# Kernel tuning notes

Measured on AMD Instinct MI355X. Metric: run time of the kernel, lower is better.

## Reference

```python
import jax, jax.numpy as jnp
import numpy as np

N_NODES = 100000
N_EDGES = 3200000
F_IN = 512
HIDDEN = 64
N_CLASSES = 64


def setup_inputs() -> dict:
    key = jax.random.key(0)
    ks = jax.random.split(key, 6)
    node_features = jax.random.normal(ks[0], (N_NODES, F_IN), dtype=jnp.float32)
    edge_rows = jax.random.randint(ks[1], (N_EDGES,), 0, N_NODES, dtype=jnp.int32)
    edge_cols = jax.random.randint(ks[2], (N_EDGES,), 0, N_NODES, dtype=jnp.int32)
    edge_vals = jax.random.uniform(ks[3], (N_EDGES,), dtype=jnp.float32)
    W1 = jax.random.normal(ks[4], (F_IN, HIDDEN), dtype=jnp.float32) / np.sqrt(F_IN)
    b1 = jnp.zeros((HIDDEN,), dtype=jnp.float32)
    W2 = jax.random.normal(ks[5], (HIDDEN, N_CLASSES), dtype=jnp.float32) / np.sqrt(HIDDEN)
    b2 = jnp.zeros((N_CLASSES,), dtype=jnp.float32)
    return {
        "node_features": node_features,
        "edge_rows": edge_rows,
        "edge_cols": edge_cols,
        "edge_vals": edge_vals,
        "W1": W1,
        "b1": b1,
        "W2": W2,
        "b2": b2,
    }


def reference(node_features, edge_rows, edge_cols, edge_vals, W1, b1, W2, b2):
    # MLP node transform (inference: dropout is identity, no norms)
    h = jax.nn.relu(node_features @ W1 + b1)          # [N, HIDDEN]
    logits = h @ W2 + b2                              # [N, C]
    # smoother @ logits : sparse [N,N] COO times dense [N,C]
    messages = edge_vals[:, None] * logits[edge_cols]  # [E, C]
    out = jax.ops.segment_sum(messages, edge_rows, num_segments=N_NODES)
    return out
```

## Files before the change

kernel.cpp:

```cpp
#include <hip/hip_runtime.h>
#include <hip/hip_bf16.h>
#include <stdint.h>

#define N_NODES 100000
#define N_EDGES 3200000
#define F_IN    512
#define HIDDEN  64
#define NCLS    64

#define BROWS   64
#define NBKT    1563
#define NBKT_PAD 1792
#define CHUNK   4096
#define CAP     2432
#define OVF_CAP 8192
#define SENTINEL ((int)0x80000000)

typedef float v4f __attribute__((ext_vector_type(4)));
typedef short v8s __attribute__((ext_vector_type(8)));

__device__ __forceinline__ unsigned short f2bf(float f){
  unsigned u = __float_as_uint(f);
  u += 0x7fffu + ((u >> 16) & 1u);
  return (unsigned short)(u >> 16);
}
__device__ __forceinline__ float bflo(unsigned u){ return __uint_as_float(u << 16); }
__device__ __forceinline__ float bfhi(unsigned u){ return __uint_as_float(u & 0xffff0000u); }

__global__ void prep_weights(const float* __restrict__ W1, const float* __restrict__ W2,
                             unsigned short* __restrict__ w1f, unsigned short* __restrict__ w2f,
                             int* __restrict__ zeroc){
  int t = blockIdx.x * 256 + threadIdx.x;
  if (t < NBKT*16 + 16) zeroc[t] = 0;
  if (t < 16*4*64*8){
    int j = t & 7, lane = (t >> 3) & 63, nt = (t >> 9) & 3, ks = t >> 11;
    int m = lane & 15, q = lane >> 4;
    int k = ks*32 + q*8 + j, n = nt*16 + m;
    w1f[t] = f2bf(W1[k*HIDDEN + n]);
  } else {
    int u = t - 16*4*64*8;
    if (u < 2*4*64*8){
      int j = u & 7, lane = (u >> 3) & 63, nt = (u >> 9) & 3, ks = u >> 11;
      int m = lane & 15, q = lane >> 4;
      int k = ks*32 + q*8 + j, n = nt*16 + m;
      w2f[u] = f2bf(W2[k*NCLS + n]);
    }
  }
}

__global__ __launch_bounds__(256) void mlp_kernel(
    const float* __restrict__ X, const float* __restrict__ b1,
    const float* __restrict__ b2,
    const unsigned short* __restrict__ w1f, const unsigned short* __restrict__ w2f,
    unsigned short* __restrict__ logits){
  __shared__ __align__(16) float lds[4][16][68];
  int tid  = threadIdx.x;
  int wid  = tid >> 6, lane = tid & 63;
  int m    = lane & 15, q = lane >> 4;
  int base = blockIdx.x * 64 + wid * 16;
  if (base > N_NODES - 16) base = N_NODES - 16;

  const float* rp = X + (size_t)(base + m) * F_IN + q * 8;
  const v8s* w1v = (const v8s*)w1f;
  const v8s* w2v = (const v8s*)w2f;

  v4f a0c = {0,0,0,0}, a1c = {0,0,0,0}, a2c = {0,0,0,0}, a3c = {0,0,0,0};
  #pragma unroll
  for (int ks = 0; ks < 16; ++ks){
    const float4* pa = (const float4*)(rp + ks * 32);
    float4 x0 = pa[0], x1 = pa[1];
    v8s af;
    af[0]=(short)f2bf(x0.x); af[1]=(short)f2bf(x0.y); af[2]=(short)f2bf(x0.z); af[3]=(short)f2bf(x0.w);
    af[4]=(short)f2bf(x1.x); af[5]=(short)f2bf(x1.y); af[6]=(short)f2bf(x1.z); af[7]=(short)f2bf(x1.w);
    a0c = __builtin_amdgcn_mfma_f32_16x16x32_bf16(af, w1v[(ks*4+0)*64 + lane], a0c, 0,0,0);
    a1c = __builtin_amdgcn_mfma_f32_16x16x32_bf16(af, w1v[(ks*4+1)*64 + lane], a1c, 0,0,0);
    a2c = __builtin_amdgcn_mfma_f32_16x16x32_bf16(af, w1v[(ks*4+2)*64 + lane], a2c, 0,0,0);
    a3c = __builtin_amdgcn_mfma_f32_16x16x32_bf16(af, w1v[(ks*4+3)*64 + lane], a3c, 0,0,0);
  }

  float b1v0 = b1[m], b1v1 = b1[16+m], b1v2 = b1[32+m], b1v3 = b1[48+m];
  #pragma unroll
  for (int r = 0; r < 4; ++r){
    int row = q*4 + r;
    lds[wid][row][     m] = fmaxf(a0c[r] + b1v0, 0.f);
    lds[wid][row][16 + m] = fmaxf(a1c[r] + b1v1, 0.f);
    lds[wid][row][32 + m] = fmaxf(a2c[r] + b1v2, 0.f);
    lds[wid][row][48 + m] = fmaxf(a3c[r] + b1v3, 0.f);
  }
  __syncthreads();

  v4f c0 = {0,0,0,0}, c1 = {0,0,0,0}, c2 = {0,0,0,0}, c3 = {0,0,0,0};
  #pragma unroll
  for (int k2 = 0; k2 < 2; ++k2){
    const float4* ph = (const float4*)&lds[wid][m][k2*32 + q*8];
    float4 h0 = ph[0], h1 = ph[1];
    v8s af;
    af[0]=(short)f2bf(h0.x); af[1]=(short)f2bf(h0.y); af[2]=(short)f2bf(h0.z); af[3]=(short)f2bf(h0.w);
    af[4]=(short)f2bf(h1.x); af[5]=(short)f2bf(h1.y); af[6]=(short)f2bf(h1.z); af[7]=(short)f2bf(h1.w);
    c0 = __builtin_amdgcn_mfma_f32_16x16x32_bf16(af, w2v[(k2*4+0)*64 + lane], c0, 0,0,0);
    c1 = __builtin_amdgcn_mfma_f32_16x16x32_bf16(af, w2v[(k2*4+1)*64 + lane], c1, 0,0,0);
    c2 = __builtin_amdgcn_mfma_f32_16x16x32_bf16(af, w2v[(k2*4+2)*64 + lane], c2, 0,0,0);
    c3 = __builtin_amdgcn_mfma_f32_16x16x32_bf16(af, w2v[(k2*4+3)*64 + lane], c3, 0,0,0);
  }

  float b2v0 = b2[m], b2v1 = b2[16+m], b2v2 = b2[32+m], b2v3 = b2[48+m];
  unsigned short* lp = logits + (size_t)base * NCLS;
  #pragma unroll
  for (int r = 0; r < 4; ++r){
    int row = q*4 + r;
    lp[row*NCLS +      m] = f2bf(c0[r] + b2v0);
    lp[row*NCLS + 16 + m] = f2bf(c1[r] + b2v1);
    lp[row*NCLS + 32 + m] = f2bf(c2[r] + b2v2);
    lp[row*NCLS + 48 + m] = f2bf(c3[r] + b2v3);
  }
}

__global__ __launch_bounds__(256) void bucket_scatter(
    const int* __restrict__ rows, const int* __restrict__ cols,
    const float* __restrict__ vals, int* __restrict__ bcur,
    int* __restrict__ ovf_cnt, int4* __restrict__ ovf,
    int2* __restrict__ ebkt){
  __shared__ int  lcnt[NBKT_PAD];
  __shared__ int  lbase[NBKT_PAD];
  __shared__ int  ssum[256];
  __shared__ int2 stage[CHUNK];
  __shared__ int  sdst[CHUNK];
  int t = threadIdx.x;
  int base = blockIdx.x * CHUNK;
  int cnt  = min(CHUNK, N_EDGES - base);

  #pragma unroll
  for (int i = 0; i < 7; ++i) lcnt[t*7 + i] = 0;
  __syncthreads();

  int r[16];
  #pragma unroll
  for (int k = 0; k < 16; ++k){
    int li = t + k*256;
    if (li < cnt){
      r[k] = rows[base + li];
      atomicAdd(&lcnt[r[k] >> 6], 1);
    } else r[k] = -1;
  }
  __syncthreads();

  int v[7]; int s = 0;
  #pragma unroll
  for (int k = 0; k < 7; ++k){ v[k] = lcnt[t*7 + k]; s += v[k]; }
  ssum[t] = s; __syncthreads();
  for (int o = 1; o < 256; o <<= 1){
    int add = (t >= o) ? ssum[t - o] : 0;
    __syncthreads();
    ssum[t] += add;
    __syncthreads();
  }
  int run = ssum[t] - s;
  #pragma unroll
  for (int k = 0; k < 7; ++k){
    int b = t*7 + k;
    if (b < NBKT){
      if (v[k]){
        int g = atomicAdd(&bcur[b*16], v[k]);
        lbase[b] = b*CAP + g - run;
      }
      lcnt[b] = run;
    }
    run += v[k];
  }
  __syncthreads();

  #pragma unroll
  for (int k = 0; k < 16; ++k){
    if (r[k] >= 0){
      int li = t + k*256;
      int c  = cols[base + li];
      float vv = vals[base + li];
      int b  = r[k] >> 6;
      int pos = atomicAdd(&lcnt[b], 1);
      int dest = lbase[b] + pos;
      if (dest < b*CAP + CAP){
        stage[pos] = make_int2(((r[k] & 63) << 17) | c, __float_as_int(vv));
        sdst[pos]  = lbase[b];
      } else {
        sdst[pos] = SENTINEL;
        int o = atomicAdd(ovf_cnt, 1);
        if (o < OVF_CAP) ovf[o] = make_int4(r[k], c, __float_as_int(vv), 0);
      }
    }
  }
  __syncthreads();

  for (int j = t; j < cnt; j += 256){
    int d = sdst[j];
    if (d != SENTINEL) ebkt[d + j] = stage[j];
  }
}

__global__ __launch_bounds__(256) void bucket_agg(
    const int* __restrict__ bcur, const int2* __restrict__ ebkt,
    const unsigned short* __restrict__ logits, float* __restrict__ out){
  __shared__ int2 sorted[CAP];
  __shared__ int  rc[BROWS];
  __shared__ int  rbase[BROWS + 1];
  __shared__ int  rcur[BROWS];
  int b = blockIdx.x, t = threadIdx.x;
  int w = t >> 6, lane = t & 63;
  int h = lane & 15, sel = lane >> 4;

  if (t < BROWS) rc[t] = 0;
  __syncthreads();

  int cnt = bcur[b * 16];
  if (cnt > CAP) cnt = CAP;
  const int2* ep = ebkt + (size_t)b * CAP;

  for (int j = t; j < cnt; j += 256){
    int x = ((const int*)ep)[2*j];
    atomicAdd(&rc[((unsigned)x) >> 17], 1);
  }
  __syncthreads();

  if (t < BROWS){
    int c = rc[t];
    int v = c;
    #pragma unroll
    for (int o = 1; o < 64; o <<= 1){
      int u = __shfl_up(v, o);
      if (lane >= o) v += u;
    }
    rbase[t + 1] = v;
    rcur[t]      = v - c;
    if (t == 0) rbase[0] = 0;
  }
  __syncthreads();

  for (int j = t; j < cnt; j += 256){
    int2 ev = ep[j];
    int pos = atomicAdd(&rcur[((unsigned)ev.x) >> 17], 1);
    sorted[pos] = ev;
  }
  __syncthreads();

  const uint2* lg = (const uint2*)logits;
  int row0 = b * BROWS;
  for (int n = w; n < BROWS; n += 4){
    int node = row0 + n;
    if (node >= N_NODES) break;
    int s = rbase[n], e = rbase[n + 1];
    float a0 = 0.f, a1 = 0.f, a2 = 0.f, a3 = 0.f;
    int i = s;
    for (; i + 16 <= e; i += 16){
      int2 e0 = sorted[i      + sel];
      int2 e1 = sorted[i + 4  + sel];
      int2 e2 = sorted[i + 8  + sel];
      int2 e3 = sorted[i + 12 + sel];
      uint2 u0 = lg[((size_t)(e0.x & 0x1FFFF) << 4) + h];
      uint2 u1 = lg[((size_t)(e1.x & 0x1FFFF) << 4) + h];
      uint2 u2 = lg[((size_t)(e2.x & 0x1FFFF) << 4) + h];
      uint2 u3 = lg[((size_t)(e3.x & 0x1FFFF) << 4) + h];
      float v0 = __int_as_float(e0.y), v1 = __int_as_float(e1.y);
      float v2 = __int_as_float(e2.y), v3 = __int_as_float(e3.y);
      a0 = fmaf(v0, bflo(u0.x), a0); a1 = fmaf(v0, bfhi(u0.x), a1);
      a2 = fmaf(v0, bflo(u0.y), a2); a3 = fmaf(v0, bfhi(u0.y), a3);
      a0 = fmaf(v1, bflo(u1.x), a0); a1 = fmaf(v1, bfhi(u1.x), a1);
      a2 = fmaf(v1, bflo(u1.y), a2); a3 = fmaf(v1, bfhi(u1.y), a3);
      a0 = fmaf(v2, bflo(u2.x), a0); a1 = fmaf(v2, bfhi(u2.x), a1);
      a2 = fmaf(v2, bflo(u2.y), a2); a3 = fmaf(v2, bfhi(u2.y), a3);
      a0 = fmaf(v3, bflo(u3.x), a0); a1 = fmaf(v3, bfhi(u3.x), a1);
      a2 = fmaf(v3, bflo(u3.y), a2); a3 = fmaf(v3, bfhi(u3.y), a3);
    }
    for (; i < e; i += 4){
      int idx = i + sel;
      int col = 0; float v = 0.f;
      if (idx < e){ int2 ev = sorted[idx]; col = ev.x & 0x1FFFF; v = __int_as_float(ev.y); }
      uint2 u = lg[((size_t)col << 4) + h];
      a0 = fmaf(v, bflo(u.x), a0); a1 = fmaf(v, bfhi(u.x), a1);
      a2 = fmaf(v, bflo(u.y), a2); a3 = fmaf(v, bfhi(u.y), a3);
    }
    a0 += __shfl_xor(a0, 16); a0 += __shfl_xor(a0, 32);
    a1 += __shfl_xor(a1, 16); a1 += __shfl_xor(a1, 32);
    a2 += __shfl_xor(a2, 16); a2 += __shfl_xor(a2, 32);
    a3 += __shfl_xor(a3, 16); a3 += __shfl_xor(a3, 32);
    if (sel == 0){
      float4* op = (float4*)(out + (size_t)node * NCLS);
      op[h] = make_float4(a0, a1, a2, a3);
    }
  }
}

__global__ __launch_bounds__(256) void ovf_apply(
    const int* __restrict__ ovf_cnt, const int4* __restrict__ ovf,
    const unsigned short* __restrict__ logits, float* __restrict__ out){
  int cnt = ovf_cnt[0];
  if (cnt > OVF_CAP) cnt = OVF_CAP;
  long total = (long)cnt * 64;
  for (long i = (long)blockIdx.x * 256 + threadIdx.x; i < total; i += (long)gridDim.x * 256){
    int e = (int)(i >> 6), c = (int)(i & 63);
    int4 ev = ovf[e];
    float lv = bflo(logits[((size_t)ev.y << 6) + c]);
    atomicAdd(&out[((size_t)ev.x << 6) + c], __int_as_float(ev.z) * lv);
  }
}

__global__ void scatter_atomic(const int* __restrict__ rows, const int* __restrict__ cols,
                               const float* __restrict__ vals,
                               const unsigned short* __restrict__ logits,
                               float* __restrict__ out){
  long g = (long)blockIdx.x * 256 + threadIdx.x;
  int e = (int)(g >> 6), c = (int)(g & 63);
  if (e < N_EDGES){
    float lv = __uint_as_float(((unsigned)logits[(size_t)cols[e] * NCLS + c]) << 16);
    atomicAdd(&out[(size_t)rows[e] * NCLS + c], vals[e] * lv);
  }
}

extern "C" void kernel_launch(void* const* d_in, const int* in_sizes, int n_in,
                              void* d_out, int out_size, void* d_ws, size_t ws_size,
                              hipStream_t stream){
  const float* X     = (const float*)d_in[0];
  const int*   erows = (const int*)  d_in[1];
  const int*   ecols = (const int*)  d_in[2];
  const float* evals = (const float*)d_in[3];
  const float* W1    = (const float*)d_in[4];
  const float* b1    = (const float*)d_in[5];
  const float* W2    = (const float*)d_in[6];
  const float* b2    = (const float*)d_in[7];
  float* out = (float*)d_out;

  char* ws = (char*)d_ws;
  size_t off = 0;
  auto alloc = [&](size_t bytes) -> char* {
    char* p = ws + off;
    off = (off + bytes + 255) & ~(size_t)255;
    return p;
  };
  unsigned short* logits = (unsigned short*)alloc((size_t)N_NODES * NCLS * 2);
  unsigned short* w1f    = (unsigned short*)alloc(16*4*64*8 * 2);
  unsigned short* w2f    = (unsigned short*)alloc(2*4*64*8 * 2);
  int*  bcur = (int*)alloc((size_t)(NBKT*16 + 16) * 4);
  int*  ovfc = bcur + NBKT*16;
  int4* ovf  = (int4*)alloc((size_t)OVF_CAP * 16);
  int2* ebkt = (int2*)alloc((size_t)NBKT * CAP * 8);
  size_t full_need = off;

  prep_weights<<<144, 256, 0, stream>>>(W1, W2, w1f, w2f, bcur);
  mlp_kernel<<<(N_NODES + 63) / 64, 256, 0, stream>>>(X, b1, b2, w1f, w2f, logits);

  if (ws_size >= full_need){
    bucket_scatter<<<(N_EDGES + CHUNK - 1) / CHUNK, 256, 0, stream>>>(
        erows, ecols, evals, bcur, ovfc, ovf, ebkt);
    bucket_agg<<<NBKT, 256, 0, stream>>>(bcur, ebkt, logits, out);
    ovf_apply<<<256, 256, 0, stream>>>(ovfc, ovf, logits, out);
  } else {
    hipMemsetAsync(out, 0, (size_t)N_NODES * NCLS * 4, stream);
    scatter_atomic<<<(int)(((long)N_EDGES * 64 + 255) / 256), 256, 0, stream>>>(
        erows, ecols, evals, logits, out);
  }
}
```

Before: 480.6 us.

## Split edge bucketing into two-level radix scatter via coarse buckets

Replaces the single-pass scatter into 1563 fine row buckets with two passes. The first pass scatters edges into 25 coarse buckets of 4096 rows; the second reads each coarse bucket and scatters into its 64 fine buckets. This cuts the per-block histogram, scan and global atomic cost, and writes in larger contiguous runs instead of many tiny fragments. In exchange the edge data makes an extra round trip through global memory, one more kernel is launched, and a larger workspace is needed.

```diff
diff --git a/kernel.cpp b/kernel.cpp
--- a/kernel.cpp
+++ b/kernel.cpp
@@ -10,11 +10,14 @@
 
 #define BROWS   64
 #define NBKT    1563
-#define NBKT_PAD 1792
 #define CHUNK   4096
 #define CAP     2432
+#define NCOARSE 25
+#define CAP1    135168
+#define C2BLKS  33
 #define OVF_CAP 8192
 #define SENTINEL ((int)0x80000000)
+#define NZERO   (NBKT*16 + NCOARSE*16 + 16)
 
 typedef float v4f __attribute__((ext_vector_type(4)));
 typedef short v8s __attribute__((ext_vector_type(8)));
@@ -31,7 +34,7 @@
                              unsigned short* __restrict__ w1f, unsigned short* __restrict__ w2f,
                              int* __restrict__ zeroc){
   int t = blockIdx.x * 256 + threadIdx.x;
-  if (t < NBKT*16 + 16) zeroc[t] = 0;
+  if (t < NZERO) zeroc[t] = 0;
   if (t < 16*4*64*8){
     int j = t & 7, lane = (t >> 3) & 63, nt = (t >> 9) & 3, ks = t >> 11;
     int m = lane & 15, q = lane >> 4;
@@ -115,22 +118,20 @@
   }
 }
 
-__global__ __launch_bounds__(256) void bucket_scatter(
+__global__ __launch_bounds__(256) void scat1(
     const int* __restrict__ rows, const int* __restrict__ cols,
-    const float* __restrict__ vals, int* __restrict__ bcur,
+    const float* __restrict__ vals, int* __restrict__ c1cur,
     int* __restrict__ ovf_cnt, int4* __restrict__ ovf,
-    int2* __restrict__ ebkt){
-  __shared__ int  lcnt[NBKT_PAD];
-  __shared__ int  lbase[NBKT_PAD];
-  __shared__ int  ssum[256];
+    int2* __restrict__ ebkt1){
+  __shared__ int  lcnt[32];
+  __shared__ int  lbase[32];
   __shared__ int2 stage[CHUNK];
   __shared__ int  sdst[CHUNK];
   int t = threadIdx.x;
   int base = blockIdx.x * CHUNK;
   int cnt  = min(CHUNK, N_EDGES - base);
 
-  #pragma unroll
-  for (int i = 0; i < 7; ++i) lcnt[t*7 + i] = 0;
+  if (t < 32) lcnt[t] = 0;
   __syncthreads();
 
   int r[16];
@@ -139,33 +140,25 @@
     int li = t + k*256;
     if (li < cnt){
       r[k] = rows[base + li];
-      atomicAdd(&lcnt[r[k] >> 6], 1);
+      atomicAdd(&lcnt[r[k] >> 12], 1);
     } else r[k] = -1;
   }
   __syncthreads();
 
-  int v[7]; int s = 0;
-  #pragma unroll
-  for (int k = 0; k < 7; ++k){ v[k] = lcnt[t*7 + k]; s += v[k]; }
-  ssum[t] = s; __syncthreads();
-  for (int o = 1; o < 256; o <<= 1){
-    int add = (t >= o) ? ssum[t - o] : 0;
-    __syncthreads();
-    ssum[t] += add;
-    __syncthreads();
-  }
-  int run = ssum[t] - s;
-  #pragma unroll
-  for (int k = 0; k < 7; ++k){
-    int b = t*7 + k;
-    if (b < NBKT){
-      if (v[k]){
-        int g = atomicAdd(&bcur[b*16], v[k]);
-        lbase[b] = b*CAP + g - run;
-      }
-      lcnt[b] = run;
-    }
-    run += v[k];
+  if (t < 32){
+    int cme = lcnt[t];
+    int v = cme;
+    #pragma unroll
+    for (int o = 1; o < 32; o <<= 1){
+      int u = __shfl_up(v, o);
+      if (t >= o) v += u;
+    }
+    int excl = v - cme;
+    if (cme){
+      int g = atomicAdd(&c1cur[t*16], cme);
+      lbase[t] = t*CAP1 + g - excl;
+    }
+    lcnt[t] = excl;
   }
   __syncthreads();
 
@@ -175,16 +168,93 @@
       int li = t + k*256;
       int c  = cols[base + li];
       float vv = vals[base + li];
-      int b  = r[k] >> 6;
+      int b  = r[k] >> 12;
       int pos = atomicAdd(&lcnt[b], 1);
       int dest = lbase[b] + pos;
-      if (dest < b*CAP + CAP){
-        stage[pos] = make_int2(((r[k] & 63) << 17) | c, __float_as_int(vv));
+      if (dest < b*CAP1 + CAP1){
+        stage[pos] = make_int2(((r[k] & 4095) << 17) | c, __float_as_int(vv));
         sdst[pos]  = lbase[b];
       } else {
         sdst[pos] = SENTINEL;
         int o = atomicAdd(ovf_cnt, 1);
         if (o < OVF_CAP) ovf[o] = make_int4(r[k], c, __float_as_int(vv), 0);
+      }
+    }
+  }
+  __syncthreads();
+
+  for (int j = t; j < cnt; j += 256){
+    int d = sdst[j];
+    if (d != SENTINEL) ebkt1[d + j] = stage[j];
+  }
+}
+
+__global__ __launch_bounds__(256) void scat2(
+    const int* __restrict__ c1cur, const int2* __restrict__ ebkt1,
+    int* __restrict__ bcur, int* __restrict__ ovf_cnt, int4* __restrict__ ovf,
+    int2* __restrict__ ebkt){
+  __shared__ int  lcnt[64];
+  __shared__ int  lbase[64];
+  __shared__ int2 stage[CHUNK];
+  __shared__ int  sdst[CHUNK];
+  int t = threadIdx.x;
+  int c = blockIdx.x / C2BLKS;
+  int k0 = blockIdx.x % C2BLKS;
+
+  int cntc = c1cur[c*16];
+  if (cntc > CAP1) cntc = CAP1;
+  int start = k0 * CHUNK;
+  if (start >= cntc) return;
+  int cnt = min(CHUNK, cntc - start);
+  const int2* src = ebkt1 + (size_t)c * CAP1 + start;
+
+  if (t < 64) lcnt[t] = 0;
+  __syncthreads();
+
+  int2 ev[16];
+  #pragma unroll
+  for (int k = 0; k < 16; ++k){
+    int li = t + k*256;
+    if (li < cnt){
+      ev[k] = src[li];
+      atomicAdd(&lcnt[(((unsigned)ev[k].x) >> 17) >> 6], 1);
+    } else ev[k].x = -1;
+  }
+  __syncthreads();
+
+  if (t < 64){
+    int cme = lcnt[t];
+    int v = cme;
+    #pragma unroll
+    for (int o = 1; o < 64; o <<= 1){
+      int u = __shfl_up(v, o);
+      if (t >= o) v += u;
+    }
+    int excl = v - cme;
+    if (cme){
+      int gb = c*64 + t;
+      int g = atomicAdd(&bcur[gb*16], cme);
+      lbase[t] = gb*CAP + g - excl;
+    }
+    lcnt[t] = excl;
+  }
+  __syncthreads();
+
+  #pragma unroll
+  for (int k = 0; k < 16; ++k){
+    if (ev[k].x >= 0){
+      unsigned x = (unsigned)ev[k].x;
+      int lr12 = (int)(x >> 17);
+      int fb   = lr12 >> 6;
+      int pos = atomicAdd(&lcnt[fb], 1);
+      int dest = lbase[fb] + pos;
+      if (dest < (c*64 + fb)*CAP + CAP){
+        stage[pos] = make_int2(((lr12 & 63) << 17) | (int)(x & 0x1FFFFu), ev[k].y);
+        sdst[pos]  = lbase[fb];
+      } else {
+        sdst[pos] = SENTINEL;
+        int o = atomicAdd(ovf_cnt, 1);
+        if (o < OVF_CAP) ovf[o] = make_int4(c*4096 + lr12, (int)(x & 0x1FFFFu), ev[k].y, 0);
       }
     }
   }
@@ -272,7 +342,7 @@
     for (; i < e; i += 4){
       int idx = i + sel;
       int col = 0; float v = 0.f;
-      if (idx < e){ int2 ev = sorted[idx]; col = ev.x & 0x1FFFF; v = __int_as_float(ev.y); }
+      if (idx < e){ int2 evv = sorted[idx]; col = evv.x & 0x1FFFF; v = __int_as_float(evv.y); }
       uint2 u = lg[((size_t)col << 4) + h];
       a0 = fmaf(v, bflo(u.x), a0); a1 = fmaf(v, bfhi(u.x), a1);
       a2 = fmaf(v, bflo(u.y), a2); a3 = fmaf(v, bfhi(u.y), a3);
@@ -337,18 +407,22 @@
   unsigned short* logits = (unsigned short*)alloc((size_t)N_NODES * NCLS * 2);
   unsigned short* w1f    = (unsigned short*)alloc(16*4*64*8 * 2);
   unsigned short* w2f    = (unsigned short*)alloc(2*4*64*8 * 2);
-  int*  bcur = (int*)alloc((size_t)(NBKT*16 + 16) * 4);
-  int*  ovfc = bcur + NBKT*16;
-  int4* ovf  = (int4*)alloc((size_t)OVF_CAP * 16);
-  int2* ebkt = (int2*)alloc((size_t)NBKT * CAP * 8);
+  int*  bcur  = (int*)alloc((size_t)NZERO * 4);
+  int*  c1cur = bcur + NBKT*16;
+  int*  ovfc  = bcur + NBKT*16 + NCOARSE*16;
+  int4* ovf   = (int4*)alloc((size_t)OVF_CAP * 16);
+  int2* ebkt1 = (int2*)alloc((size_t)NCOARSE * CAP1 * 8);
+  int2* ebkt  = (int2*)alloc((size_t)NBKT * CAP * 8);
   size_t full_need = off;
 
   prep_weights<<<144, 256, 0, stream>>>(W1, W2, w1f, w2f, bcur);
   mlp_kernel<<<(N_NODES + 63) / 64, 256, 0, stream>>>(X, b1, b2, w1f, w2f, logits);
 
   if (ws_size >= full_need){
-    bucket_scatter<<<(N_EDGES + CHUNK - 1) / CHUNK, 256, 0, stream>>>(
-        erows, ecols, evals, bcur, ovfc, ovf, ebkt);
+    scat1<<<(N_EDGES + CHUNK - 1) / CHUNK, 256, 0, stream>>>(
+        erows, ecols, evals, c1cur, ovfc, ovf, ebkt1);
+    scat2<<<NCOARSE * C2BLKS, 256, 0, stream>>>(
+        c1cur, ebkt1, bcur, ovfc, ovf, ebkt);
     bucket_agg<<<NBKT, 256, 0, stream>>>(bcur, ebkt, logits, out);
     ovf_apply<<<256, 256, 0, stream>>>(ovfc, ovf, logits, out);
   } else {
```

Result: faster. 451.0 us (-6.2%).
